# Performance work log

Hardware: AMD Instinct MI355X
Metric: run time of the kernel (lower is better)

The kernel has to match this reference:

```python
import jax, jax.numpy as jnp
import numpy as np

EPS = 1.1920929e-07  # torch.finfo(float32).eps, used by F.rms_norm default

def rope(x, cos, sin):
    # x: [B,T,H,D]; cos/sin: [1,T,1,D//2]
    d = x.shape[-1] // 2
    x1, x2 = x[..., :d], x[..., d:]
    return jnp.concatenate([x1 * cos + x2 * sin, -x1 * sin + x2 * cos], axis=-1)

def rmsnorm(x):
    return x * jax.lax.rsqrt(jnp.mean(x * x, axis=-1, keepdims=True) + EPS)

def setup_inputs() -> dict:
    key = jax.random.key(0)
    ks = jax.random.split(key, 9)
    B, T, E = 2, 2048, 1024
    Hkv, D = 4, 64
    return {
        "x": jax.random.normal(ks[0], (B, T, E), jnp.float32),
        "ve": jax.random.normal(ks[1], (B, T, Hkv * D), jnp.float32),
        "cos": jax.random.normal(ks[2], (1, T, 1, D // 2), jnp.float32),
        "sin": jax.random.normal(ks[3], (1, T, 1, D // 2), jnp.float32),
        "Wq": jax.random.normal(ks[4], (E, E), jnp.float32) * 0.02,
        "Wk": jax.random.normal(ks[5], (Hkv * D, E), jnp.float32) * 0.02,
        "Wv": jax.random.normal(ks[6], (Hkv * D, E), jnp.float32) * 0.02,
        "Wproj": jax.random.normal(ks[7], (E, E), jnp.float32) * 0.02,
        "Wgate": jax.random.normal(ks[8], (Hkv, 32), jnp.float32) * 0.02,
        "window_size": 1024,
    }

def reference(x, ve, cos, sin, Wq, Wk, Wv, Wproj, Wgate, window_size):
    B, T, E = x.shape
    H, Hkv, D = 16, 4, 64
    G = H // Hkv  # GQA group size
    q = (x @ Wq.T).reshape(B, T, H, D)
    k = (x @ Wk.T).reshape(B, T, Hkv, D)
    v = (x @ Wv.T).reshape(B, T, Hkv, D)
    # value-embedding gating
    gate = 2.0 * jax.nn.sigmoid(x[..., :32] @ Wgate.T)          # [B,T,Hkv]
    v = v + gate[..., None] * ve.reshape(B, T, Hkv, D)
    # RoPE then QK RMS-norm
    q = rmsnorm(rope(q, cos, sin))
    k = rmsnorm(rope(k, cos, sin))
    # to [B,H,T,D]; repeat-interleave kv heads for GQA (matches torch enable_gqa)
    q = q.transpose(0, 2, 1, 3)
    k = jnp.repeat(k.transpose(0, 2, 1, 3), G, axis=1)
    v = jnp.repeat(v.transpose(0, 2, 1, 3), G, axis=1)
    # causal + sliding-window boolean mask
    row = jnp.arange(T)[:, None]
    col = jnp.arange(T)[None, :]
    mask = (col <= row) & (col >= row - window_size)            # [T,T]
    scale = 1.0 / jnp.sqrt(jnp.float32(D))
    scores = jnp.einsum("bhqd,bhkd->bhqk", q, k) * scale
    scores = jnp.where(mask, scores, -jnp.inf)
    p = jax.nn.softmax(scores, axis=-1)
    y = jnp.einsum("bhqk,bhkd->bhqd", p, v)
    y = y.transpose(0, 2, 1, 3).reshape(B, T, E)
    return y @ Wproj.T
```

## Files before the change

kernel.cpp:

```cpp
#include <hip/hip_runtime.h>


typedef float f32x4 __attribute__((ext_vector_type(4)));
typedef short s16x8 __attribute__((ext_vector_type(8)));
typedef short s16x4 __attribute__((ext_vector_type(4)));
typedef _Float16 f16x4 __attribute__((ext_vector_type(4)));

__device__ __forceinline__ unsigned short f2bf(float f) {
  unsigned u = __float_as_uint(f);
  u += 0x7fffu + ((u >> 16) & 1u);
  return (unsigned short)(u >> 16);
}
__device__ __forceinline__ unsigned short h16(float f) {
  _Float16 h = (_Float16)f;
  return __builtin_bit_cast(unsigned short, h);
}

__device__ __forceinline__ float fexp2(float x) {
#if __has_builtin(__builtin_amdgcn_exp2f)
  return __builtin_amdgcn_exp2f(x);
#else
  return __expf(x * 0.69314718f);
#endif
}

__device__ __forceinline__ void gl2lds16(const unsigned short* g, unsigned short* l) {
  __builtin_amdgcn_global_load_lds((const __attribute__((address_space(1))) unsigned int*)g,
                                   (__attribute__((address_space(3))) unsigned int*)l, 16, 0, 0);
}

__global__ __launch_bounds__(256) void cvt_all(
    const float* __restrict__ x, const float* __restrict__ wq, const float* __restrict__ wk,
    const float* __restrict__ wv, const float* __restrict__ wp,
    unsigned short* __restrict__ xb, unsigned short* __restrict__ wqkv,
    unsigned short* __restrict__ wpj) {
  int i = blockIdx.x * 256 + threadIdx.x;
  const float* s;
  unsigned short* d;
  if (i < 1048576) { s = x; d = xb; }
  else if (i < 1310720) { i -= 1048576; s = wq; d = wqkv; }
  else if (i < 1376256) { i -= 1310720; s = wk; d = wqkv + 1048576; }
  else if (i < 1441792) { i -= 1376256; s = wv; d = wqkv + 1310720; }
  else { i -= 1441792; s = wp; d = wpj; }
  float4 v = ((const float4*)s)[i];
  ushort4 o;
  o.x = f2bf(v.x); o.y = f2bf(v.y); o.z = f2bf(v.z); o.w = f2bf(v.w);
  ((ushort4*)d)[i] = o;
}

__global__ __launch_bounds__(256) void gate_kernel(const float* __restrict__ x,
                                                   const float* __restrict__ wgate,
                                                   float* __restrict__ gatep) {
  int i = blockIdx.x * 256 + threadIdx.x;
  int bt = i >> 2, h = i & 3;
  const float4* xp = (const float4*)(x + (size_t)bt * 1024);
  const float4* wp = (const float4*)(wgate + h * 32);
  float s = 0.f;
#pragma unroll
  for (int j = 0; j < 8; ++j) {
    float4 a = xp[j], b = wp[j];
    s += a.x * b.x + a.y * b.y + a.z * b.z + a.w * b.w;
  }
  gatep[i] = 2.f / (1.f + __expf(-s));
}

__global__ __launch_bounds__(256) void gemm_qkv(
    const unsigned short* __restrict__ A, const unsigned short* __restrict__ B,
    const float* __restrict__ cosp, const float* __restrict__ sinp,
    const float* __restrict__ gatep, const float* __restrict__ ve,
    unsigned short* __restrict__ q_r, unsigned short* __restrict__ k_r,
    unsigned short* __restrict__ v_r) {
  __shared__ unsigned short As[128 * 32];
  __shared__ unsigned short Bs[128 * 32];
  const int K = 1024;
  int bn = blockIdx.x, bm = blockIdx.y;
  int t = threadIdx.x;
  int w = t >> 6, lane = t & 63;
  int c = lane & 15, g = lane >> 4;
  int wm = w >> 1, wn = w & 1;

  f32x4 acc[4][4];
#pragma unroll
  for (int i = 0; i < 4; ++i)
#pragma unroll
    for (int j = 0; j < 4; ++j) acc[i][j] = (f32x4){0.f, 0.f, 0.f, 0.f};

  const unsigned short* Ab = A + (size_t)(bm * 128) * K;
  const unsigned short* Bb = B + (size_t)(bn * 128) * K;
  int srow = lane >> 2;
  int scol = (lane & 3) * 8;

  for (int k0 = 0; k0 < K; k0 += 32) {
#pragma unroll
    for (int j = 0; j < 2; ++j) {
      int rbase = j * 64 + w * 16;
      gl2lds16(Ab + (size_t)(rbase + srow) * K + k0 + scol, As + rbase * 32);
      gl2lds16(Bb + (size_t)(rbase + srow) * K + k0 + scol, Bs + rbase * 32);
    }
    __syncthreads();
    s16x8 af[4], bf[4];
#pragma unroll
    for (int mt = 0; mt < 4; ++mt)
      af[mt] = *(const s16x8*)(As + (wm * 64 + mt * 16 + c) * 32 + g * 8);
#pragma unroll
    for (int nt = 0; nt < 4; ++nt)
      bf[nt] = *(const s16x8*)(Bs + (wn * 64 + nt * 16 + c) * 32 + g * 8);
#pragma unroll
    for (int mt = 0; mt < 4; ++mt)
#pragma unroll
      for (int nt = 0; nt < 4; ++nt)
        acc[mt][nt] = __builtin_amdgcn_mfma_f32_16x16x32_bf16(af[mt], bf[nt], acc[mt][nt], 0, 0, 0);
    __syncthreads();
  }

  const float QSCL = 0.125f * 1.44269504f;
#pragma unroll
  for (int mt = 0; mt < 4; ++mt) {
#pragma unroll
    for (int r = 0; r < 4; ++r) {
      int row = bm * 128 + wm * 64 + mt * 16 + g * 4 + r;
      int b = row >> 11, tt = row & 2047;
      float v0 = acc[mt][0][r], v1 = acc[mt][1][r], v2 = acc[mt][2][r], v3 = acc[mt][3][r];
      if (bn < 10) {
        float cs0 = cosp[tt * 32 + c], sn0 = sinp[tt * 32 + c];
        float cs1 = cosp[tt * 32 + 16 + c], sn1 = sinp[tt * 32 + 16 + c];
        float r0 = v0 * cs0 + v2 * sn0;
        float r1 = v1 * cs1 + v3 * sn1;
        float r2 = v2 * cs0 - v0 * sn0;
        float r3 = v3 * cs1 - v1 * sn1;
        float ss = r0 * r0 + r1 * r1 + r2 * r2 + r3 * r3;
        ss += __shfl_xor(ss, 1);
        ss += __shfl_xor(ss, 2);
        ss += __shfl_xor(ss, 4);
        ss += __shfl_xor(ss, 8);
        float sc = rsqrtf(ss * (1.0f / 64.0f) + 1.1920929e-07f);
        if (bn < 8) {
          int h = bn * 2 + wn;
          unsigned short* qp = q_r + ((size_t)(b * 16 + h) * 2048 + tt) * 64;
          float s2 = sc * QSCL;
          qp[c] = f2bf(r0 * s2);
          qp[16 + c] = f2bf(r1 * s2);
          qp[32 + c] = f2bf(r2 * s2);
          qp[48 + c] = f2bf(r3 * s2);
        } else {
          int h = (bn - 8) * 2 + wn;
          unsigned short* kp = k_r + ((size_t)(b * 4 + h) * 2048 + tt) * 64;
          kp[c] = f2bf(r0 * sc);
          kp[16 + c] = f2bf(r1 * sc);
          kp[32 + c] = f2bf(r2 * sc);
          kp[48 + c] = f2bf(r3 * sc);
        }
      } else {
        int h = (bn - 10) * 2 + wn;
        float gate = gatep[row * 4 + h];
        const float* vep = ve + (size_t)row * 256 + h * 64;
        unsigned short* vp = v_r + ((size_t)(b * 4 + h) * 2048 + tt) * 64;
        vp[c] = h16(v0 + gate * vep[c]);
        vp[16 + c] = h16(v1 + gate * vep[16 + c]);
        vp[32 + c] = h16(v2 + gate * vep[32 + c]);
        vp[48 + c] = h16(v3 + gate * vep[48 + c]);
      }
    }
  }
}

__global__ __launch_bounds__(256) void gemm_bf16_64(
    const unsigned short* __restrict__ A, const unsigned short* __restrict__ B,
    float* __restrict__ C, int K, int ldc) {
  __shared__ unsigned short As[64 * 32];
  __shared__ unsigned short Bs[128 * 32];
  int bn = blockIdx.x, bm = blockIdx.y;
  int t = threadIdx.x;
  int w = t >> 6, lane = t & 63;
  int c = lane & 15, g = lane >> 4;
  int wm = w >> 1, wn = w & 1;

  f32x4 acc[2][4];
#pragma unroll
  for (int i = 0; i < 2; ++i)
#pragma unroll
    for (int j = 0; j < 4; ++j) acc[i][j] = (f32x4){0.f, 0.f, 0.f, 0.f};

  const unsigned short* Ab = A + (size_t)(bm * 64) * K;
  const unsigned short* Bb = B + (size_t)(bn * 128) * K;
  int srow = lane >> 2;
  int scol = (lane & 3) * 8;

  for (int k0 = 0; k0 < K; k0 += 32) {
    gl2lds16(Ab + (size_t)(w * 16 + srow) * K + k0 + scol, As + w * 512);
    gl2lds16(Bb + (size_t)(w * 16 + srow) * K + k0 + scol, Bs + w * 512);
    gl2lds16(Bb + (size_t)(64 + w * 16 + srow) * K + k0 + scol, Bs + 2048 + w * 512);
    __syncthreads();
    s16x8 af[2], bf[4];
#pragma unroll
    for (int mt = 0; mt < 2; ++mt)
      af[mt] = *(const s16x8*)(As + (wm * 32 + mt * 16 + c) * 32 + g * 8);
#pragma unroll
    for (int nt = 0; nt < 4; ++nt)
      bf[nt] = *(const s16x8*)(Bs + (wn * 64 + nt * 16 + c) * 32 + g * 8);
#pragma unroll
    for (int mt = 0; mt < 2; ++mt)
#pragma unroll
      for (int nt = 0; nt < 4; ++nt)
        acc[mt][nt] = __builtin_amdgcn_mfma_f32_16x16x32_bf16(af[mt], bf[nt], acc[mt][nt], 0, 0, 0);
    __syncthreads();
  }
#pragma unroll
  for (int mt = 0; mt < 2; ++mt)
#pragma unroll
    for (int nt = 0; nt < 4; ++nt)
#pragma unroll
      for (int r = 0; r < 4; ++r) {
        int rowg = bm * 64 + wm * 32 + mt * 16 + g * 4 + r;
        int colg = bn * 128 + wn * 64 + nt * 16 + c;
        C[(size_t)rowg * ldc + colg] = acc[mt][nt][r];
      }
}

__global__ __launch_bounds__(256) void transpose_v(const unsigned short* __restrict__ v_r,
                                                   unsigned short* __restrict__ v_p2) {
  __shared__ unsigned short tile[64][72];
  int blk = blockIdx.x;
  int s = blk >> 5;
  int t0 = (blk & 31) * 64;
  int tt = threadIdx.x;
  int rcol = (tt & 7) * 8;
  int rrow = tt >> 3;
#pragma unroll
  for (int i = 0; i < 2; ++i) {
    int row = rrow + i * 32;
    *(s16x8*)&tile[row][rcol] = *(const s16x8*)(v_r + ((size_t)s * 2048 + t0 + row) * 64 + rcol);
  }
  __syncthreads();
#pragma unroll
  for (int i = 0; i < 2; ++i) {
    int idx = tt + i * 256;
    int ht = idx >> 8;
    int d = (idx >> 2) & 63;
    int e8 = (idx & 3) * 8;
    s16x8 o;
#pragma unroll
    for (int j = 0; j < 8; ++j) o[j] = tile[ht * 32 + e8 + j][d];
    *(s16x8*)(v_p2 + (size_t)s * 131072 + ((size_t)((t0 >> 5) + ht)) * 2048 + d * 32 + e8) = o;
  }
}

__global__ __launch_bounds__(256) void attn_kernel(
    const unsigned short* __restrict__ q_r, const unsigned short* __restrict__ k_r,
    const unsigned short* __restrict__ v_p2, unsigned short* __restrict__ y_b,
    const int* __restrict__ wptr) {
  const int W = *wptr;
  const int bid = blockIdx.x;
  const int qt = bid & 31, h = (bid >> 5) & 15, b = bid >> 9;
  const int tid = threadIdx.x;
  const int w = tid >> 6, lane = tid & 63, c = lane & 15, g = lane >> 4;
  const int r0b = qt * 64;
  const int r0w = r0b + w * 16;
  const int hkv = h >> 2;
  const float M = 11.5415603f;

  __shared__ unsigned short Ks[32 * 68];
  __shared__ unsigned short Vs[64 * 40];

  const unsigned short* kbase = k_r + (size_t)(b * 4 + hkv) * 131072;
  const unsigned short* vbase = v_p2 + (size_t)(b * 4 + hkv) * 131072;
  const unsigned short* qbase = q_r + ((size_t)(b * 16 + h) * 2048 + r0w) * 64;

  s16x8 q_lo = *(const s16x8*)(qbase + c * 64 + g * 8);
  s16x8 q_hi = *(const s16x8*)(qbase + c * 64 + 32 + g * 8);

  int kt0w = r0w - W; if (kt0w < 0) kt0w = 0;
  const int ktEw = r0w + 16;
  int KT0 = r0b - W; if (KT0 < 0) KT0 = 0;
  KT0 &= ~31;
  const int KTE = r0b + 64;

  float l_part = 0.f;
  f32x4 acc[4];
#pragma unroll
  for (int dt = 0; dt < 4; ++dt) acc[dt] = (f32x4){0.f, 0.f, 0.f, 0.f};

  s16x8 pk = *(const s16x8*)(kbase + (size_t)KT0 * 64 + tid * 8);
  s16x8 pv = *(const s16x8*)(vbase + (size_t)(KT0 >> 5) * 2048 + tid * 8);

  unsigned short* kdst = Ks + (tid >> 3) * 68 + (tid & 7) * 8;
  unsigned short* vdst = Vs + (tid >> 2) * 40 + (tid & 3) * 8;

  for (int kt = KT0; kt < KTE; kt += 32) {
    int nkt = (kt + 32 < KTE) ? kt + 32 : kt;
    s16x8 nk = *(const s16x8*)(kbase + (size_t)nkt * 64 + tid * 8);
    s16x8 nv = *(const s16x8*)(vbase + (size_t)(nkt >> 5) * 2048 + tid * 8);

    *(s16x4*)kdst = __builtin_shufflevector(pk, pk, 0, 1, 2, 3);
    *(s16x4*)(kdst + 4) = __builtin_shufflevector(pk, pk, 4, 5, 6, 7);
    *(s16x8*)vdst = pv;
    __syncthreads();

    if (kt + 32 > kt0w && kt < ktEw) {
      const unsigned short* kr0 = Ks + c * 68 + g * 8;
      s16x4 a0 = *(const s16x4*)(kr0);
      s16x4 a1 = *(const s16x4*)(kr0 + 4);
      s16x4 a2 = *(const s16x4*)(kr0 + 32);
      s16x4 a3 = *(const s16x4*)(kr0 + 36);
      const unsigned short* kr1 = kr0 + 16 * 68;
      s16x4 a4 = *(const s16x4*)(kr1);
      s16x4 a5 = *(const s16x4*)(kr1 + 4);
      s16x4 a6 = *(const s16x4*)(kr1 + 32);
      s16x4 a7 = *(const s16x4*)(kr1 + 36);
      s16x8 k0lo = __builtin_shufflevector(a0, a1, 0, 1, 2, 3, 4, 5, 6, 7);
      s16x8 k0hi = __builtin_shufflevector(a2, a3, 0, 1, 2, 3, 4, 5, 6, 7);
      s16x8 k1lo = __builtin_shufflevector(a4, a5, 0, 1, 2, 3, 4, 5, 6, 7);
      s16x8 k1hi = __builtin_shufflevector(a6, a7, 0, 1, 2, 3, 4, 5, 6, 7);

      f32x4 S0 = (f32x4){0.f, 0.f, 0.f, 0.f};
      f32x4 S1 = (f32x4){0.f, 0.f, 0.f, 0.f};
      S0 = __builtin_amdgcn_mfma_f32_16x16x32_bf16(k0lo, q_lo, S0, 0, 0, 0);
      S0 = __builtin_amdgcn_mfma_f32_16x16x32_bf16(k0hi, q_hi, S0, 0, 0, 0);
      S1 = __builtin_amdgcn_mfma_f32_16x16x32_bf16(k1lo, q_lo, S1, 0, 0, 0);
      S1 = __builtin_amdgcn_mfma_f32_16x16x32_bf16(k1hi, q_hi, S1, 0, 0, 0);

      f16x4 P0, P1;
      const bool edge = (kt < kt0w + 32) || (kt + 32 > r0w);
      const int qrow = r0w + c;
#pragma unroll
      for (int r = 0; r < 4; ++r) {
        float p0 = fexp2(S0[r] - M);
        float p1 = fexp2(S1[r] - M);
        if (edge) {
          int k0i = kt + g * 4 + r;
          int k1i = k0i + 16;
          if (!(k0i <= qrow && k0i >= qrow - W)) p0 = 0.f;
          if (!(k1i <= qrow && k1i >= qrow - W)) p1 = 0.f;
        }
        l_part += p0 + p1;
        P0[r] = (_Float16)p0;
        P1[r] = (_Float16)p1;
      }

#pragma unroll
      for (int dt = 0; dt < 4; ++dt) {
        const unsigned short* vr = Vs + (dt * 16 + c) * 40 + g * 4;
        f16x4 va = *(const f16x4*)(vr);
        f16x4 vb = *(const f16x4*)(vr + 16);
        acc[dt] = __builtin_amdgcn_mfma_f32_16x16x16f16(va, P0, acc[dt], 0, 0, 0);
        acc[dt] = __builtin_amdgcn_mfma_f32_16x16x16f16(vb, P1, acc[dt], 0, 0, 0);
      }
    }
    __syncthreads();
    pk = nk; pv = nv;
  }

  float l = l_part;
  l += __shfl_xor(l, 16);
  l += __shfl_xor(l, 32);
  float inv = 1.0f / l;

  unsigned short* ob = y_b + ((size_t)(b * 2048 + r0w + c) * 16 + h) * 64 + g * 4;
#pragma unroll
  for (int dt = 0; dt < 4; ++dt) {
    ushort4 o;
    o.x = f2bf(acc[dt][0] * inv);
    o.y = f2bf(acc[dt][1] * inv);
    o.z = f2bf(acc[dt][2] * inv);
    o.w = f2bf(acc[dt][3] * inv);
    *(ushort4*)(ob + dt * 16) = o;
  }
}

extern "C" void kernel_launch(void* const* d_in, const int* in_sizes, int n_in,
                              void* d_out, int out_size, void* d_ws, size_t ws_size,
                              hipStream_t stream) {
  const float* x = (const float*)d_in[0];
  const float* ve = (const float*)d_in[1];
  const float* cosp = (const float*)d_in[2];
  const float* sinp = (const float*)d_in[3];
  const float* Wq = (const float*)d_in[4];
  const float* Wk = (const float*)d_in[5];
  const float* Wv = (const float*)d_in[6];
  const float* Wproj = (const float*)d_in[7];
  const float* Wgate = (const float*)d_in[8];
  const int* wptr = (const int*)d_in[9];

  unsigned short* xb = (unsigned short*)d_ws;
  unsigned short* wqkv = xb + 4194304;
  unsigned short* wpj = wqkv + 1572864;
  unsigned short* q_r = wpj + 1048576;
  unsigned short* k_r = q_r + 4194304;
  unsigned short* v_r = k_r + 1048576;
  unsigned short* y_b = v_r + 1048576;
  unsigned short* vp2 = y_b + 4194304;
  float* gatep = (float*)(vp2 + 1048576);

  cvt_all<<<6656, 256, 0, stream>>>(x, Wq, Wk, Wv, Wproj, xb, wqkv, wpj);
  gate_kernel<<<64, 256, 0, stream>>>(x, Wgate, gatep);
  gemm_qkv<<<dim3(12, 32), 256, 0, stream>>>(xb, wqkv, cosp, sinp, gatep, ve, q_r, k_r, v_r);
  transpose_v<<<256, 256, 0, stream>>>(v_r, vp2);
  attn_kernel<<<1024, 256, 0, stream>>>(q_r, k_r, vp2, y_b, wptr);
  gemm_bf16_64<<<dim3(8, 64), 256, 0, stream>>>(y_b, wpj, (float*)d_out, 1024, 1024);
}
```

Measured before the change: 191.8 us.

## Halve QKV GEMM M-tile and double-buffer 64-key attention tiles

The QKV GEMM block tile drops from 128 to 64 rows and the grid doubles (12x64 blocks), which raises block count and occupancy at the cost of reloading B tiles more often. The attention kernel now stages 64-key K/V tiles into double-buffered shared memory, which removes one __syncthreads per iteration. It processes four 16-key sub-tiles and skips sub-tiles that fall outside each wave's window. The trade-off is more LDS use and a new V layout (stride 72) in exchange for fewer barriers and less wasted masked work.

Measured after the change: 204.8 us. 6.8% more time.

```diff
diff --git a/kernel.cpp b/kernel.cpp
--- a/kernel.cpp
+++ b/kernel.cpp
@@ -70,7 +70,7 @@
     const float* __restrict__ gatep, const float* __restrict__ ve,
     unsigned short* __restrict__ q_r, unsigned short* __restrict__ k_r,
     unsigned short* __restrict__ v_r) {
-  __shared__ unsigned short As[128 * 32];
+  __shared__ unsigned short As[64 * 32];
   __shared__ unsigned short Bs[128 * 32];
   const int K = 1024;
   int bn = blockIdx.x, bm = blockIdx.y;
@@ -79,34 +79,31 @@
   int c = lane & 15, g = lane >> 4;
   int wm = w >> 1, wn = w & 1;
 
-  f32x4 acc[4][4];
-#pragma unroll
-  for (int i = 0; i < 4; ++i)
+  f32x4 acc[2][4];
+#pragma unroll
+  for (int i = 0; i < 2; ++i)
 #pragma unroll
     for (int j = 0; j < 4; ++j) acc[i][j] = (f32x4){0.f, 0.f, 0.f, 0.f};
 
-  const unsigned short* Ab = A + (size_t)(bm * 128) * K;
+  const unsigned short* Ab = A + (size_t)(bm * 64) * K;
   const unsigned short* Bb = B + (size_t)(bn * 128) * K;
   int srow = lane >> 2;
   int scol = (lane & 3) * 8;
 
   for (int k0 = 0; k0 < K; k0 += 32) {
-#pragma unroll
-    for (int j = 0; j < 2; ++j) {
-      int rbase = j * 64 + w * 16;
-      gl2lds16(Ab + (size_t)(rbase + srow) * K + k0 + scol, As + rbase * 32);
-      gl2lds16(Bb + (size_t)(rbase + srow) * K + k0 + scol, Bs + rbase * 32);
-    }
+    gl2lds16(Ab + (size_t)(w * 16 + srow) * K + k0 + scol, As + w * 512);
+    gl2lds16(Bb + (size_t)(w * 16 + srow) * K + k0 + scol, Bs + w * 512);
+    gl2lds16(Bb + (size_t)(64 + w * 16 + srow) * K + k0 + scol, Bs + 2048 + w * 512);
     __syncthreads();
-    s16x8 af[4], bf[4];
-#pragma unroll
-    for (int mt = 0; mt < 4; ++mt)
-      af[mt] = *(const s16x8*)(As + (wm * 64 + mt * 16 + c) * 32 + g * 8);
+    s16x8 af[2], bf[4];
+#pragma unroll
+    for (int mt = 0; mt < 2; ++mt)
+      af[mt] = *(const s16x8*)(As + (wm * 32 + mt * 16 + c) * 32 + g * 8);
 #pragma unroll
     for (int nt = 0; nt < 4; ++nt)
       bf[nt] = *(const s16x8*)(Bs + (wn * 64 + nt * 16 + c) * 32 + g * 8);
 #pragma unroll
-    for (int mt = 0; mt < 4; ++mt)
+    for (int mt = 0; mt < 2; ++mt)
 #pragma unroll
       for (int nt = 0; nt < 4; ++nt)
         acc[mt][nt] = __builtin_amdgcn_mfma_f32_16x16x32_bf16(af[mt], bf[nt], acc[mt][nt], 0, 0, 0);
@@ -115,10 +112,10 @@
 
   const float QSCL = 0.125f * 1.44269504f;
 #pragma unroll
-  for (int mt = 0; mt < 4; ++mt) {
+  for (int mt = 0; mt < 2; ++mt) {
 #pragma unroll
     for (int r = 0; r < 4; ++r) {
-      int row = bm * 128 + wm * 64 + mt * 16 + g * 4 + r;
+      int row = bm * 64 + wm * 32 + mt * 16 + g * 4 + r;
       int b = row >> 11, tt = row & 2047;
       float v0 = acc[mt][0][r], v1 = acc[mt][1][r], v2 = acc[mt][2][r], v3 = acc[mt][3][r];
       if (bn < 10) {
@@ -259,8 +256,8 @@
   const int hkv = h >> 2;
   const float M = 11.5415603f;
 
-  __shared__ unsigned short Ks[32 * 68];
-  __shared__ unsigned short Vs[64 * 40];
+  __shared__ unsigned short Ks[2][64 * 68];
+  __shared__ unsigned short Vs[2][64 * 72];
 
   const unsigned short* kbase = k_r + (size_t)(b * 4 + hkv) * 131072;
   const unsigned short* vbase = v_p2 + (size_t)(b * 4 + hkv) * 131072;
@@ -272,82 +269,86 @@
   int kt0w = r0w - W; if (kt0w < 0) kt0w = 0;
   const int ktEw = r0w + 16;
   int KT0 = r0b - W; if (KT0 < 0) KT0 = 0;
-  KT0 &= ~31;
+  KT0 &= ~63;
   const int KTE = r0b + 64;
+  const int nst = (KTE - KT0) >> 6;
+
+  const int krow = tid >> 2;
+  const int kcol = (tid & 3) * 16;
+  const int vtile = tid >> 7;
+  const int vd = (tid >> 1) & 63;
+  const int vk0 = (tid & 1) * 16;
 
   float l_part = 0.f;
   f32x4 acc[4];
 #pragma unroll
   for (int dt = 0; dt < 4; ++dt) acc[dt] = (f32x4){0.f, 0.f, 0.f, 0.f};
 
-  s16x8 pk = *(const s16x8*)(kbase + (size_t)KT0 * 64 + tid * 8);
-  s16x8 pv = *(const s16x8*)(vbase + (size_t)(KT0 >> 5) * 2048 + tid * 8);
-
-  unsigned short* kdst = Ks + (tid >> 3) * 68 + (tid & 7) * 8;
-  unsigned short* vdst = Vs + (tid >> 2) * 40 + (tid & 3) * 8;
-
-  for (int kt = KT0; kt < KTE; kt += 32) {
-    int nkt = (kt + 32 < KTE) ? kt + 32 : kt;
-    s16x8 nk = *(const s16x8*)(kbase + (size_t)nkt * 64 + tid * 8);
-    s16x8 nv = *(const s16x8*)(vbase + (size_t)(nkt >> 5) * 2048 + tid * 8);
-
-    *(s16x4*)kdst = __builtin_shufflevector(pk, pk, 0, 1, 2, 3);
-    *(s16x4*)(kdst + 4) = __builtin_shufflevector(pk, pk, 4, 5, 6, 7);
-    *(s16x8*)vdst = pv;
+  s16x8 pk0, pk1, pv0, pv1;
+  {
+    const unsigned short* kg = kbase + (size_t)(KT0 + krow) * 64 + kcol;
+    pk0 = *(const s16x8*)kg; pk1 = *(const s16x8*)(kg + 8);
+    const unsigned short* vg = vbase + (size_t)((KT0 >> 5) + vtile) * 2048 + vd * 32 + vk0;
+    pv0 = *(const s16x8*)vg; pv1 = *(const s16x8*)(vg + 8);
+  }
+
+  for (int s = 0; s < nst; ++s) {
+    const int kt = KT0 + (s << 6);
+    const int nkt = (s + 1 < nst) ? kt + 64 : kt;
+    s16x8 nk0, nk1, nv0, nv1;
+    {
+      const unsigned short* kg = kbase + (size_t)(nkt + krow) * 64 + kcol;
+      nk0 = *(const s16x8*)kg; nk1 = *(const s16x8*)(kg + 8);
+      const unsigned short* vg = vbase + (size_t)((nkt >> 5) + vtile) * 2048 + vd * 32 + vk0;
+      nv0 = *(const s16x8*)vg; nv1 = *(const s16x8*)(vg + 8);
+    }
+
+    unsigned short* kd = &Ks[s & 1][krow * 68 + kcol];
+    *(s16x8*)kd = pk0; *(s16x8*)(kd + 8) = pk1;
+    unsigned short* vdp = &Vs[s & 1][vd * 72 + vtile * 32 + vk0];
+    *(s16x8*)vdp = pv0; *(s16x8*)(vdp + 8) = pv1;
     __syncthreads();
 
-    if (kt + 32 > kt0w && kt < ktEw) {
-      const unsigned short* kr0 = Ks + c * 68 + g * 8;
-      s16x4 a0 = *(const s16x4*)(kr0);
-      s16x4 a1 = *(const s16x4*)(kr0 + 4);
-      s16x4 a2 = *(const s16x4*)(kr0 + 32);
-      s16x4 a3 = *(const s16x4*)(kr0 + 36);
-      const unsigned short* kr1 = kr0 + 16 * 68;
-      s16x4 a4 = *(const s16x4*)(kr1);
-      s16x4 a5 = *(const s16x4*)(kr1 + 4);
-      s16x4 a6 = *(const s16x4*)(kr1 + 32);
-      s16x4 a7 = *(const s16x4*)(kr1 + 36);
-      s16x8 k0lo = __builtin_shufflevector(a0, a1, 0, 1, 2, 3, 4, 5, 6, 7);
-      s16x8 k0hi = __builtin_shufflevector(a2, a3, 0, 1, 2, 3, 4, 5, 6, 7);
-      s16x8 k1lo = __builtin_shufflevector(a4, a5, 0, 1, 2, 3, 4, 5, 6, 7);
-      s16x8 k1hi = __builtin_shufflevector(a6, a7, 0, 1, 2, 3, 4, 5, 6, 7);
-
-      f32x4 S0 = (f32x4){0.f, 0.f, 0.f, 0.f};
-      f32x4 S1 = (f32x4){0.f, 0.f, 0.f, 0.f};
-      S0 = __builtin_amdgcn_mfma_f32_16x16x32_bf16(k0lo, q_lo, S0, 0, 0, 0);
-      S0 = __builtin_amdgcn_mfma_f32_16x16x32_bf16(k0hi, q_hi, S0, 0, 0, 0);
-      S1 = __builtin_amdgcn_mfma_f32_16x16x32_bf16(k1lo, q_lo, S1, 0, 0, 0);
-      S1 = __builtin_amdgcn_mfma_f32_16x16x32_bf16(k1hi, q_hi, S1, 0, 0, 0);
-
-      f16x4 P0, P1;
-      const bool edge = (kt < kt0w + 32) || (kt + 32 > r0w);
-      const int qrow = r0w + c;
-#pragma unroll
-      for (int r = 0; r < 4; ++r) {
-        float p0 = fexp2(S0[r] - M);
-        float p1 = fexp2(S1[r] - M);
-        if (edge) {
-          int k0i = kt + g * 4 + r;
-          int k1i = k0i + 16;
-          if (!(k0i <= qrow && k0i >= qrow - W)) p0 = 0.f;
-          if (!(k1i <= qrow && k1i >= qrow - W)) p1 = 0.f;
+    if (kt + 64 > kt0w && kt < ktEw) {
+      const unsigned short* Kb = &Ks[s & 1][0];
+      const unsigned short* Vb = &Vs[s & 1][0];
+#pragma unroll
+      for (int ks = 0; ks < 4; ++ks) {
+        const int kb = kt + ks * 16;
+        if (kb >= ktEw || kb + 16 <= kt0w) continue;
+        const unsigned short* kr = Kb + (ks * 16 + c) * 68 + g * 8;
+        s16x4 a0 = *(const s16x4*)(kr);
+        s16x4 a1 = *(const s16x4*)(kr + 4);
+        s16x4 a2 = *(const s16x4*)(kr + 32);
+        s16x4 a3 = *(const s16x4*)(kr + 36);
+        s16x8 klo = __builtin_shufflevector(a0, a1, 0, 1, 2, 3, 4, 5, 6, 7);
+        s16x8 khi = __builtin_shufflevector(a2, a3, 0, 1, 2, 3, 4, 5, 6, 7);
+
+        f32x4 S = (f32x4){0.f, 0.f, 0.f, 0.f};
+        S = __builtin_amdgcn_mfma_f32_16x16x32_bf16(klo, q_lo, S, 0, 0, 0);
+        S = __builtin_amdgcn_mfma_f32_16x16x32_bf16(khi, q_hi, S, 0, 0, 0);
+
+        const bool edge = (kb < kt0w + 16) || (kb + 16 > r0w);
+        const int qrow = r0w + c;
+        f16x4 P;
+#pragma unroll
+        for (int r = 0; r < 4; ++r) {
+          float p = fexp2(S[r] - M);
+          if (edge) {
+            int ki = kb + g * 4 + r;
+            if (!(ki <= qrow && ki >= qrow - W)) p = 0.f;
+          }
+          l_part += p;
+          P[r] = (_Float16)p;
         }
-        l_part += p0 + p1;
-        P0[r] = (_Float16)p0;
-        P1[r] = (_Float16)p1;
-      }
-
-#pragma unroll
-      for (int dt = 0; dt < 4; ++dt) {
-        const unsigned short* vr = Vs + (dt * 16 + c) * 40 + g * 4;
-        f16x4 va = *(const f16x4*)(vr);
-        f16x4 vb = *(const f16x4*)(vr + 16);
-        acc[dt] = __builtin_amdgcn_mfma_f32_16x16x16f16(va, P0, acc[dt], 0, 0, 0);
-        acc[dt] = __builtin_amdgcn_mfma_f32_16x16x16f16(vb, P1, acc[dt], 0, 0, 0);
+#pragma unroll
+        for (int dt = 0; dt < 4; ++dt) {
+          f16x4 va = *(const f16x4*)(Vb + (dt * 16 + c) * 72 + ks * 16 + g * 4);
+          acc[dt] = __builtin_amdgcn_mfma_f32_16x16x16f16(va, P, acc[dt], 0, 0, 0);
+        }
       }
     }
-    __syncthreads();
-    pk = nk; pv = nv;
+    pk0 = nk0; pk1 = nk1; pv0 = nv0; pv1 = nv1;
   }
 
   float l = l_part;
@@ -393,7 +394,7 @@
 
   cvt_all<<<6656, 256, 0, stream>>>(x, Wq, Wk, Wv, Wproj, xb, wqkv, wpj);
   gate_kernel<<<64, 256, 0, stream>>>(x, Wgate, gatep);
-  gemm_qkv<<<dim3(12, 32), 256, 0, stream>>>(xb, wqkv, cosp, sinp, gatep, ve, q_r, k_r, v_r);
+  gemm_qkv<<<dim3(12, 64), 256, 0, stream>>>(xb, wqkv, cosp, sinp, gatep, ve, q_r, k_r, v_r);
   transpose_v<<<256, 256, 0, stream>>>(v_r, vp2);
   attn_kernel<<<1024, 256, 0, stream>>>(q_r, k_r, vp2, y_b, wptr);
   gemm_bf16_64<<<dim3(8, 64), 256, 0, stream>>>(y_b, wpj, (float*)d_out, 1024, 1024);
```

## Halve QKV GEMM M-tile, stage Q/K epilogue via LDS, fuse gate into convert

Applied to the files above, without the earlier changes.

The gate computation is merged into the bf16 conversion kernel, saving one launch. The QKV GEMM tile shrinks from 128 to 64 rows, doubling the grid to 768 blocks so more CUs are busy. The Q/K epilogue now writes RoPE+RMSNorm results into a per-wave LDS buffer and then emits 16-byte vector stores instead of scattered 2-byte stores. The cost is lower reuse of B per block, extra LDS, and reliance on an lgkmcnt wait rather than a barrier for the intra-wave LDS handoff.

Measured after the change: 185.8 us. 1.03x faster.

```diff
diff --git a/kernel.cpp b/kernel.cpp
--- a/kernel.cpp
+++ b/kernel.cpp
@@ -29,39 +29,38 @@
                                    (__attribute__((address_space(3))) unsigned int*)l, 16, 0, 0);
 }
 
-__global__ __launch_bounds__(256) void cvt_all(
+__global__ __launch_bounds__(256) void cvt_gate(
     const float* __restrict__ x, const float* __restrict__ wq, const float* __restrict__ wk,
-    const float* __restrict__ wv, const float* __restrict__ wp,
+    const float* __restrict__ wv, const float* __restrict__ wp, const float* __restrict__ wgate,
     unsigned short* __restrict__ xb, unsigned short* __restrict__ wqkv,
-    unsigned short* __restrict__ wpj) {
-  int i = blockIdx.x * 256 + threadIdx.x;
-  const float* s;
-  unsigned short* d;
-  if (i < 1048576) { s = x; d = xb; }
-  else if (i < 1310720) { i -= 1048576; s = wq; d = wqkv; }
-  else if (i < 1376256) { i -= 1310720; s = wk; d = wqkv + 1048576; }
-  else if (i < 1441792) { i -= 1376256; s = wv; d = wqkv + 1310720; }
-  else { i -= 1441792; s = wp; d = wpj; }
-  float4 v = ((const float4*)s)[i];
-  ushort4 o;
-  o.x = f2bf(v.x); o.y = f2bf(v.y); o.z = f2bf(v.z); o.w = f2bf(v.w);
-  ((ushort4*)d)[i] = o;
-}
-
-__global__ __launch_bounds__(256) void gate_kernel(const float* __restrict__ x,
-                                                   const float* __restrict__ wgate,
-                                                   float* __restrict__ gatep) {
-  int i = blockIdx.x * 256 + threadIdx.x;
-  int bt = i >> 2, h = i & 3;
-  const float4* xp = (const float4*)(x + (size_t)bt * 1024);
-  const float4* wp = (const float4*)(wgate + h * 32);
-  float s = 0.f;
-#pragma unroll
-  for (int j = 0; j < 8; ++j) {
-    float4 a = xp[j], b = wp[j];
-    s += a.x * b.x + a.y * b.y + a.z * b.z + a.w * b.w;
-  }
-  gatep[i] = 2.f / (1.f + __expf(-s));
+    unsigned short* __restrict__ wpj, float* __restrict__ gatep) {
+  int blk = blockIdx.x;
+  if (blk < 6656) {
+    int i = blk * 256 + threadIdx.x;
+    const float* s;
+    unsigned short* d;
+    if (i < 1048576) { s = x; d = xb; }
+    else if (i < 1310720) { i -= 1048576; s = wq; d = wqkv; }
+    else if (i < 1376256) { i -= 1310720; s = wk; d = wqkv + 1048576; }
+    else if (i < 1441792) { i -= 1376256; s = wv; d = wqkv + 1310720; }
+    else { i -= 1441792; s = wp; d = wpj; }
+    float4 v = ((const float4*)s)[i];
+    ushort4 o;
+    o.x = f2bf(v.x); o.y = f2bf(v.y); o.z = f2bf(v.z); o.w = f2bf(v.w);
+    ((ushort4*)d)[i] = o;
+  } else {
+    int i = (blk - 6656) * 256 + threadIdx.x;
+    int bt = i >> 2, h = i & 3;
+    const float4* xp = (const float4*)(x + (size_t)bt * 1024);
+    const float4* wpt = (const float4*)(wgate + h * 32);
+    float s = 0.f;
+#pragma unroll
+    for (int j = 0; j < 8; ++j) {
+      float4 a = xp[j], b = wpt[j];
+      s += a.x * b.x + a.y * b.y + a.z * b.z + a.w * b.w;
+    }
+    gatep[i] = 2.f / (1.f + __expf(-s));
+  }
 }
 
 __global__ __launch_bounds__(256) void gemm_qkv(
@@ -70,8 +69,9 @@
     const float* __restrict__ gatep, const float* __restrict__ ve,
     unsigned short* __restrict__ q_r, unsigned short* __restrict__ k_r,
     unsigned short* __restrict__ v_r) {
-  __shared__ unsigned short As[128 * 32];
+  __shared__ unsigned short As[64 * 32];
   __shared__ unsigned short Bs[128 * 32];
+  __shared__ unsigned short epi[4][32 * 68];
   const int K = 1024;
   int bn = blockIdx.x, bm = blockIdx.y;
   int t = threadIdx.x;
@@ -79,34 +79,31 @@
   int c = lane & 15, g = lane >> 4;
   int wm = w >> 1, wn = w & 1;
 
-  f32x4 acc[4][4];
-#pragma unroll
-  for (int i = 0; i < 4; ++i)
+  f32x4 acc[2][4];
+#pragma unroll
+  for (int i = 0; i < 2; ++i)
 #pragma unroll
     for (int j = 0; j < 4; ++j) acc[i][j] = (f32x4){0.f, 0.f, 0.f, 0.f};
 
-  const unsigned short* Ab = A + (size_t)(bm * 128) * K;
+  const unsigned short* Ab = A + (size_t)(bm * 64) * K;
   const unsigned short* Bb = B + (size_t)(bn * 128) * K;
   int srow = lane >> 2;
   int scol = (lane & 3) * 8;
 
   for (int k0 = 0; k0 < K; k0 += 32) {
-#pragma unroll
-    for (int j = 0; j < 2; ++j) {
-      int rbase = j * 64 + w * 16;
-      gl2lds16(Ab + (size_t)(rbase + srow) * K + k0 + scol, As + rbase * 32);
-      gl2lds16(Bb + (size_t)(rbase + srow) * K + k0 + scol, Bs + rbase * 32);
-    }
-    __syncthreads();
-    s16x8 af[4], bf[4];
-#pragma unroll
-    for (int mt = 0; mt < 4; ++mt)
-      af[mt] = *(const s16x8*)(As + (wm * 64 + mt * 16 + c) * 32 + g * 8);
+    gl2lds16(Ab + (size_t)(w * 16 + srow) * K + k0 + scol, As + w * 512);
+    gl2lds16(Bb + (size_t)(w * 16 + srow) * K + k0 + scol, Bs + w * 512);
+    gl2lds16(Bb + (size_t)(64 + w * 16 + srow) * K + k0 + scol, Bs + 2048 + w * 512);
+    __syncthreads();
+    s16x8 af[2], bf[4];
+#pragma unroll
+    for (int mt = 0; mt < 2; ++mt)
+      af[mt] = *(const s16x8*)(As + (wm * 32 + mt * 16 + c) * 32 + g * 8);
 #pragma unroll
     for (int nt = 0; nt < 4; ++nt)
       bf[nt] = *(const s16x8*)(Bs + (wn * 64 + nt * 16 + c) * 32 + g * 8);
 #pragma unroll
-    for (int mt = 0; mt < 4; ++mt)
+    for (int mt = 0; mt < 2; ++mt)
 #pragma unroll
       for (int nt = 0; nt < 4; ++nt)
         acc[mt][nt] = __builtin_amdgcn_mfma_f32_16x16x32_bf16(af[mt], bf[nt], acc[mt][nt], 0, 0, 0);
@@ -114,14 +111,16 @@
   }
 
   const float QSCL = 0.125f * 1.44269504f;
-#pragma unroll
-  for (int mt = 0; mt < 4; ++mt) {
-#pragma unroll
-    for (int r = 0; r < 4; ++r) {
-      int row = bm * 128 + wm * 64 + mt * 16 + g * 4 + r;
-      int b = row >> 11, tt = row & 2047;
-      float v0 = acc[mt][0][r], v1 = acc[mt][1][r], v2 = acc[mt][2][r], v3 = acc[mt][3][r];
-      if (bn < 10) {
+  if (bn < 10) {
+    unsigned short* eb = epi[w];
+#pragma unroll
+    for (int mt = 0; mt < 2; ++mt) {
+#pragma unroll
+      for (int r = 0; r < 4; ++r) {
+        int lrow = mt * 16 + g * 4 + r;
+        int rowg = bm * 64 + wm * 32 + lrow;
+        int tt = rowg & 2047;
+        float v0 = acc[mt][0][r], v1 = acc[mt][1][r], v2 = acc[mt][2][r], v3 = acc[mt][3][r];
         float cs0 = cosp[tt * 32 + c], sn0 = sinp[tt * 32 + c];
         float cs1 = cosp[tt * 32 + 16 + c], sn1 = sinp[tt * 32 + 16 + c];
         float r0 = v0 * cs0 + v2 * sn0;
@@ -134,31 +133,42 @@
         ss += __shfl_xor(ss, 4);
         ss += __shfl_xor(ss, 8);
         float sc = rsqrtf(ss * (1.0f / 64.0f) + 1.1920929e-07f);
-        if (bn < 8) {
-          int h = bn * 2 + wn;
-          unsigned short* qp = q_r + ((size_t)(b * 16 + h) * 2048 + tt) * 64;
-          float s2 = sc * QSCL;
-          qp[c] = f2bf(r0 * s2);
-          qp[16 + c] = f2bf(r1 * s2);
-          qp[32 + c] = f2bf(r2 * s2);
-          qp[48 + c] = f2bf(r3 * s2);
-        } else {
-          int h = (bn - 8) * 2 + wn;
-          unsigned short* kp = k_r + ((size_t)(b * 4 + h) * 2048 + tt) * 64;
-          kp[c] = f2bf(r0 * sc);
-          kp[16 + c] = f2bf(r1 * sc);
-          kp[32 + c] = f2bf(r2 * sc);
-          kp[48 + c] = f2bf(r3 * sc);
-        }
-      } else {
+        if (bn < 8) sc *= QSCL;
+        eb[lrow * 68 + c] = f2bf(r0 * sc);
+        eb[lrow * 68 + 16 + c] = f2bf(r1 * sc);
+        eb[lrow * 68 + 32 + c] = f2bf(r2 * sc);
+        eb[lrow * 68 + 48 + c] = f2bf(r3 * sc);
+      }
+    }
+    asm volatile("s_waitcnt lgkmcnt(0)" ::: "memory");
+#pragma unroll
+    for (int j = 0; j < 4; ++j) {
+      int idx = lane * 4 + j;
+      int lrow = idx >> 3;
+      int ck = idx & 7;
+      s16x8 val = *(const s16x8*)(eb + lrow * 68 + ck * 8);
+      int rowg = bm * 64 + wm * 32 + lrow;
+      int b = rowg >> 11, tt = rowg & 2047;
+      unsigned short* dst;
+      if (bn < 8) dst = q_r + ((size_t)(b * 16 + bn * 2 + wn) * 2048 + tt) * 64 + ck * 8;
+      else dst = k_r + ((size_t)(b * 4 + (bn - 8) * 2 + wn) * 2048 + tt) * 64 + ck * 8;
+      *(s16x8*)dst = val;
+    }
+  } else {
+#pragma unroll
+    for (int mt = 0; mt < 2; ++mt) {
+#pragma unroll
+      for (int r = 0; r < 4; ++r) {
+        int rowg = bm * 64 + wm * 32 + mt * 16 + g * 4 + r;
+        int b = rowg >> 11, tt = rowg & 2047;
         int h = (bn - 10) * 2 + wn;
-        float gate = gatep[row * 4 + h];
-        const float* vep = ve + (size_t)row * 256 + h * 64;
+        float gate = gatep[rowg * 4 + h];
+        const float* vep = ve + (size_t)rowg * 256 + h * 64;
         unsigned short* vp = v_r + ((size_t)(b * 4 + h) * 2048 + tt) * 64;
-        vp[c] = h16(v0 + gate * vep[c]);
-        vp[16 + c] = h16(v1 + gate * vep[16 + c]);
-        vp[32 + c] = h16(v2 + gate * vep[32 + c]);
-        vp[48 + c] = h16(v3 + gate * vep[48 + c]);
+        vp[c] = h16(acc[mt][0][r] + gate * vep[c]);
+        vp[16 + c] = h16(acc[mt][1][r] + gate * vep[16 + c]);
+        vp[32 + c] = h16(acc[mt][2][r] + gate * vep[32 + c]);
+        vp[48 + c] = h16(acc[mt][3][r] + gate * vep[48 + c]);
       }
     }
   }
@@ -391,9 +401,8 @@
   unsigned short* vp2 = y_b + 4194304;
   float* gatep = (float*)(vp2 + 1048576);
 
-  cvt_all<<<6656, 256, 0, stream>>>(x, Wq, Wk, Wv, Wproj, xb, wqkv, wpj);
-  gate_kernel<<<64, 256, 0, stream>>>(x, Wgate, gatep);
-  gemm_qkv<<<dim3(12, 32), 256, 0, stream>>>(xb, wqkv, cosp, sinp, gatep, ve, q_r, k_r, v_r);
+  cvt_gate<<<6720, 256, 0, stream>>>(x, Wq, Wk, Wv, Wproj, Wgate, xb, wqkv, wpj, gatep);
+  gemm_qkv<<<dim3(12, 64), 256, 0, stream>>>(xb, wqkv, cosp, sinp, gatep, ve, q_r, k_r, v_r);
   transpose_v<<<256, 256, 0, stream>>>(v_r, vp2);
   attn_kernel<<<1024, 256, 0, stream>>>(q_r, k_r, vp2, y_b, wptr);
   gemm_bf16_64<<<dim3(8, 64), 256, 0, stream>>>(y_b, wpj, (float*)d_out, 1024, 1024);
```
